# Performance work log

Measured on AMD Instinct MI355X. Metric: run time of the kernel, lower is better.

The kernel has to match this reference:

```python
import jax, jax.numpy as jnp
import numpy as np

N_EMBD = 1024
N_HEAD = 16
HEAD_SIZE = 64
EPS = 1e-5


def _layer_norm(x, gamma, beta, eps=EPS):
    mu = jnp.mean(x, axis=-1, keepdims=True)
    var = jnp.mean(jnp.square(x - mu), axis=-1, keepdims=True)
    return (x - mu) * jax.lax.rsqrt(var + eps) * gamma + beta


def setup_inputs() -> dict:
    key = jax.random.key(0)
    ks = jax.random.split(key, 10)
    C = N_EMBD
    s = 1.0 / np.sqrt(C)
    x = jax.random.normal(ks[0], (4, 2048, C), dtype=jnp.float32)
    Wq = jax.random.normal(ks[1], (C, C), dtype=jnp.float32) * s
    Wk = jax.random.normal(ks[2], (C, C), dtype=jnp.float32) * s
    Wv = jax.random.normal(ks[3], (C, C), dtype=jnp.float32) * s
    Wo = jax.random.normal(ks[4], (C, C), dtype=jnp.float32) * s
    W1 = jax.random.normal(ks[5], (C, 4 * C), dtype=jnp.float32) * s
    b1 = jnp.zeros((4 * C,), dtype=jnp.float32)
    W2 = jax.random.normal(ks[6], (4 * C, C), dtype=jnp.float32) * (1.0 / np.sqrt(4 * C))
    b2 = jnp.zeros((C,), dtype=jnp.float32)
    g1 = jnp.ones((C,), dtype=jnp.float32)
    be1 = jnp.zeros((C,), dtype=jnp.float32)
    g2 = jnp.ones((C,), dtype=jnp.float32)
    be2 = jnp.zeros((C,), dtype=jnp.float32)
    return {"x": x, "Wq": Wq, "Wk": Wk, "Wv": Wv, "Wo": Wo,
            "W1": W1, "b1": b1, "W2": W2, "b2": b2,
            "g1": g1, "be1": be1, "g2": g2, "be2": be2}


def _block(x, Wq, Wk, Wv, Wo, W1, b1, W2, b2, g1, be1, g2, be2):
    B, T, C = x.shape
    H, D = N_HEAD, HEAD_SIZE
    # attention sub-block
    h = _layer_norm(x, g1, be1)
    q = (h @ Wq.T).reshape(B, T, H, D).transpose(0, 2, 1, 3)  # [B,H,T,D]
    k = (h @ Wk.T).reshape(B, T, H, D).transpose(0, 2, 1, 3)
    v = (h @ Wv.T).reshape(B, T, H, D).transpose(0, 2, 1, 3)
    wei = jnp.einsum("bhqd,bhkd->bhqk", q, k) * (D ** -0.5)
    causal = jnp.tril(jnp.ones((T, T), dtype=bool))
    wei = jnp.where(causal, wei, -jnp.inf)
    wei = jax.nn.softmax(wei, axis=-1)
    out = jnp.einsum("bhqk,bhkd->bhqd", wei, v)
    out = out.transpose(0, 2, 1, 3).reshape(B, T, C)
    x = x + out @ Wo.T
    # FFN sub-block (exact erf GELU, matching torch default)
    h2 = _layer_norm(x, g2, be2)
    ff = jax.nn.gelu(h2 @ W1 + b1, approximate=False) @ W2 + b2
    return x + ff


def reference(x, Wq, Wk, Wv, Wo, W1, b1, W2, b2, g1, be1, g2, be2):
    return _block(x, Wq, Wk, Wv, Wo, W1, b1, W2, b2, g1, be1, g2, be2)
```

## Files before the change

### kernel.cpp

```cpp
#include <hip/hip_runtime.h>
#include <cmath>

typedef unsigned short u16;
typedef __attribute__((ext_vector_type(8))) short bf16x8;
typedef __attribute__((ext_vector_type(4))) float f32x4;

#define TT 2048
#define CC 1024
#define BT 8192

__device__ __forceinline__ float fexp2(float x) {
  return __builtin_amdgcn_exp2f(x);
}

__device__ __forceinline__ u16 f2bf(float f) {
  unsigned u = __builtin_bit_cast(unsigned, f);
  u += 0x7fffu + ((u >> 16) & 1u);
  return (u16)(u >> 16);
}

__device__ __forceinline__ float bf2f(u16 u) {
  return __builtin_bit_cast(float, (unsigned)u << 16);
}

__device__ __forceinline__ float gelu_tanh(float v) {
  float u2 = v * (1.595769122f + 0.071354816f * v * v);
  return v / (1.f + __expf(-u2));
}

__device__ __forceinline__ void gload_lds16(const void* g, void* l) {
  __builtin_amdgcn_global_load_lds(
      (const __attribute__((address_space(1))) void*)g,
      (__attribute__((address_space(3))) void*)l, 16, 0, 0);
}


__global__ __launch_bounds__(256) void cvt_kernel(const float* __restrict__ s,
                                                  u16* __restrict__ d) {
  int i = (blockIdx.x * 256 + threadIdx.x) * 4;
  float4 v = *(const float4*)(s + i);
  ushort4 o;
  o.x = f2bf(v.x); o.y = f2bf(v.y); o.z = f2bf(v.z); o.w = f2bf(v.w);
  *(ushort4*)(d + i) = o;
}

__global__ __launch_bounds__(256) void transpose_cvt(const float* __restrict__ src,
                                                     u16* __restrict__ dst,
                                                     int R, int C) {
  __shared__ float tile[32][33];
  int c0 = blockIdx.x * 32, r0 = blockIdx.y * 32;
  int tx = threadIdx.x, ty = threadIdx.y;
#pragma unroll
  for (int j = 0; j < 4; ++j)
    tile[ty + j * 8][tx] = src[(size_t)(r0 + ty + j * 8) * C + c0 + tx];
  __syncthreads();
#pragma unroll
  for (int j = 0; j < 4; ++j)
    dst[(size_t)(c0 + ty + j * 8) * R + r0 + tx] = f2bf(tile[tx][ty + j * 8]);
}


__global__ __launch_bounds__(256) void ln_kernel(const float* __restrict__ x,
                                                 const float* __restrict__ gw,
                                                 const float* __restrict__ bw,
                                                 u16* __restrict__ out) {
  int row = blockIdx.x;
  int tid = threadIdx.x;
  const size_t base = (size_t)row * CC;
  float4 v = *(const float4*)(x + base + tid * 4);
  float s = v.x + v.y + v.z + v.w;
  float q = v.x * v.x + v.y * v.y + v.z * v.z + v.w * v.w;
#pragma unroll
  for (int o = 32; o > 0; o >>= 1) {
    s += __shfl_down(s, o, 64);
    q += __shfl_down(q, o, 64);
  }
  __shared__ float red[8];
  __shared__ float stat[2];
  int lane = tid & 63, wid = tid >> 6;
  if (!lane) { red[wid] = s; red[4 + wid] = q; }
  __syncthreads();
  if (!tid) {
    float S = red[0] + red[1] + red[2] + red[3];
    float Q = red[4] + red[5] + red[6] + red[7];
    float mu = S * (1.0f / CC);
    float var = Q * (1.0f / CC) - mu * mu;
    stat[0] = mu;
    stat[1] = rsqrtf(var + 1e-5f);
  }
  __syncthreads();
  float mu = stat[0], rs = stat[1];
  int c = tid * 4;
  float4 gv = *(const float4*)(gw + c);
  float4 bv = *(const float4*)(bw + c);
  ushort4 o;
  o.x = f2bf((v.x - mu) * rs * gv.x + bv.x);
  o.y = f2bf((v.y - mu) * rs * gv.y + bv.y);
  o.z = f2bf((v.z - mu) * rs * gv.z + bv.z);
  o.w = f2bf((v.w - mu) * rs * gv.w + bv.w);
  *(ushort4*)(out + base + c) = o;
}


__global__ __launch_bounds__(256) void rf2_kernel(const u16* __restrict__ p0,
                                                  const u16* __restrict__ p1,
                                                  const float* __restrict__ b2,
                                                  const float* __restrict__ resid,
                                                  float* __restrict__ out) {
  int c = threadIdx.x * 4;
  size_t i = (size_t)blockIdx.x * CC + c;
  ushort4 a = *(const ushort4*)(p0 + i);
  ushort4 b = *(const ushort4*)(p1 + i);
  float4 r = *(const float4*)(resid + i);
  float4 bb = *(const float4*)(b2 + c);
  float4 o;
  o.x = bf2f(a.x) + bf2f(b.x) + r.x + bb.x;
  o.y = bf2f(a.y) + bf2f(b.y) + r.y + bb.y;
  o.z = bf2f(a.z) + bf2f(b.z) + r.z + bb.z;
  o.w = bf2f(a.w) + bf2f(b.w) + r.w + bb.w;
  *(float4*)(out + i) = o;
}


template <int EPI>
__global__ __launch_bounds__(512) void gemm256(const u16* __restrict__ A,
                                               const u16* __restrict__ B,
                                               void* __restrict__ Cv,
                                               const float* __restrict__ bias,
                                               const float* __restrict__ resid,
                                               u16* __restrict__ vt,
                                               int N, int K, int Kst,
                                               int gn, int kdiv) {
  __shared__ u16 lds[8][8192];
  const int tid = threadIdx.x, lane = tid & 63, wid = tid >> 6;
  const int nwg = gridDim.x;
  const int bid = blockIdx.x;
  const int sb = (nwg & 7) ? bid : ((bid & 7) * (nwg >> 3) + (bid >> 3));
  const int kslice = sb / kdiv, rem = sb % kdiv;
  const int tM = (rem / gn) * 256, tN = (rem % gn) * 256;
  const int wm = wid >> 2, wn = wid & 3;
  const int fr = lane & 15, g4 = lane >> 4;
  const int gsw = (g4 ^ ((fr >> 3) << 1)) * 8;
  const int srow0 = wid * 16 + (lane >> 2);
  const int scol = ((lane & 3) ^ ((lane >> 5) << 1)) * 8;
  const u16* pA = A + (size_t)kslice * K + (size_t)tM * Kst + (size_t)srow0 * Kst + scol;
  const u16* pB = B + (size_t)kslice * K + (size_t)tN * Kst + (size_t)srow0 * Kst + scol;
  const int NKT = K >> 6;
  f32x4 acc[8][4] = {};

  auto stage = [&](int idx) {
    int kof = (idx >> 1) << 5;
    const u16* G = (idx & 1) ? pB : pA;
    u16* dst = &lds[idx & 7][wid * 512];
    gload_lds16(G + kof, dst);
    gload_lds16(G + (size_t)128 * Kst + kof, dst + 4096);
  };

#pragma unroll
  for (int j = 0; j < 4; ++j) stage(j);
  asm volatile("s_waitcnt vmcnt(4)" ::: "memory");
#pragma unroll
  for (int j = 4; j < 7; ++j) stage(j);
  asm volatile("s_waitcnt vmcnt(6)" ::: "memory");
  __builtin_amdgcn_s_barrier();

  for (int t2 = 0; t2 < NKT; t2 += 2) {
#pragma unroll
    for (int tt = 0; tt < 2; ++tt) {
      const int t = t2 + tt;
      const int bo = tt << 2;
#pragma unroll
      for (int ks = 0; ks < 2; ++ks) {
        const u16* Ah = lds[bo | (ks << 1)];
        const u16* Bh = lds[bo | (ks << 1) | 1];
        bf16x8 bfr[4];
#pragma unroll
        for (int ni = 0; ni < 4; ++ni)
          bfr[ni] = *(const bf16x8*)&Bh[(wn * 64 + ni * 16 + fr) * 32 + gsw];
#pragma unroll
        for (int mh = 0; mh < 2; ++mh) {
          bf16x8 af[4];
#pragma unroll
          for (int mi = 0; mi < 4; ++mi)
            af[mi] = *(const bf16x8*)&Ah[(wm * 128 + mh * 64 + mi * 16 + fr) * 32 + gsw];
          __builtin_amdgcn_sched_barrier(0);
          int idx = 4 * t + (ks << 1) + mh + 7;
          if (idx < 4 * NKT) stage(idx);
          __builtin_amdgcn_s_barrier();
          asm volatile("s_waitcnt lgkmcnt(0)" ::: "memory");
          __builtin_amdgcn_sched_barrier(0);
          __builtin_amdgcn_s_setprio(1);
#pragma unroll
          for (int mi = 0; mi < 4; ++mi)
#pragma unroll
            for (int ni = 0; ni < 4; ++ni)
              acc[mh * 4 + mi][ni] = __builtin_amdgcn_mfma_f32_16x16x32_bf16(
                  af[mi], bfr[ni], acc[mh * 4 + mi][ni], 0, 0, 0);
          __builtin_amdgcn_s_setprio(0);
          __builtin_amdgcn_sched_barrier(0);
          if (ks == 1 && mh == 1) {
            if (t < NKT - 2) asm volatile("s_waitcnt vmcnt(6)" ::: "memory");
            else if (t == NKT - 2) asm volatile("s_waitcnt vmcnt(0)" ::: "memory");
          }
          __builtin_amdgcn_s_barrier();
        }
      }
    }
  }

#pragma unroll
  for (int m = 0; m < 8; ++m) {
#pragma unroll
    for (int ni = 0; ni < 4; ++ni) {
      const int gR0 = tM + wm * 128 + m * 16 + g4 * 4;
      const int gC = tN + wn * 64 + ni * 16 + fr;
      if constexpr (EPI == 4) {
        if (gC < 2048) {
          float sc = (gC < 1024) ? 0.180336884f : 1.0f;
#pragma unroll
          for (int r = 0; r < 4; ++r)
            ((u16*)Cv)[(size_t)(gR0 + r) * 3072 + gC] = f2bf(acc[m][ni][r] * sc);
        } else {
          int tr = gR0 & 2047, bb = gR0 >> 11;
          int dv = gC - 2048, hh = dv >> 6, dd = dv & 63;
          int k5 = tr & 31;
          int pos = ((k5 & 15) >> 2) * 8 + ((k5 >> 4) & 1) * 4;
          ushort4 q4;
          q4.x = f2bf(acc[m][ni][0]);
          q4.y = f2bf(acc[m][ni][1]);
          q4.z = f2bf(acc[m][ni][2]);
          q4.w = f2bf(acc[m][ni][3]);
          *(ushort4*)&vt[((size_t)((bb * 16 + hh) * 64 + dd)) * 2048 + (tr & ~31) + pos] = q4;
        }
      } else if constexpr (EPI == 0) {
        u16* dst = kslice ? vt : (u16*)Cv;
#pragma unroll
        for (int r = 0; r < 4; ++r)
          dst[(size_t)(gR0 + r) * N + gC] = f2bf(acc[m][ni][r]);
      } else if constexpr (EPI == 2) {
#pragma unroll
        for (int r = 0; r < 4; ++r) {
          float v = gelu_tanh(acc[m][ni][r] + bias[gC]);
          ((u16*)Cv)[(size_t)(gR0 + r) * N + gC] = f2bf(v);
        }
      } else {
#pragma unroll
        for (int r = 0; r < 4; ++r) {
          size_t idx = (size_t)(gR0 + r) * N + gC;
          float v = acc[m][ni][r] + resid[idx];
          if constexpr (EPI == 3) v += bias[gC];
          ((float*)Cv)[idx] = v;
        }
      }
    }
  }
}


__global__ __launch_bounds__(256) void attn_kernel(const u16* __restrict__ qkv,
                                                   const u16* __restrict__ vt,
                                                   u16* __restrict__ out) {
  const int bid = blockIdx.x;
  const int sb = (bid & 7) * 128 + (bid >> 3);
  const int pair = sb & 15;
  const int bh = sb >> 4;
  const int b = bh >> 4, h = bh & 15;
  const int tid = threadIdx.x, lane = tid & 63, wid = tid >> 6;
  const int ql = lane & 15, g = lane >> 4;
  const int sw = ql & 7;
  __shared__ u16 Ks[2][4096];
  __shared__ u16 Vs[2][4096];
  const size_t rowQbase = (size_t)b * TT;
  const u16* kpart = qkv + rowQbase * 3072 + 1024 + h * 64;
  const u16* vpart = vt + ((size_t)(b * 16 + h) * 64) * 2048;
  const int srow = lane >> 3;
  const int sc16 = lane & 7;

  for (int pass = 0; pass < 2; ++pass) {
    const int qt = pass ? (31 - pair) : pair;
    const int qrow0 = qt * 64 + wid * 16;
    const int q_glb = qrow0 + ql;
    const u16* qp = qkv + (rowQbase + q_glb) * 3072 + h * 64 + g * 8;
    bf16x8 qf0 = *(const bf16x8*)qp;
    bf16x8 qf1 = *(const bf16x8*)(qp + 32);
    f32x4 o[4] = {};
    float m_run = -1e30f, l_run = 0.f;
    const int nt = qt + 1;

    auto stage = [&](int bufi, int t) {
      int kv0 = t * 64;
#pragma unroll
      for (int i = 0; i < 2; ++i) {
        int seg = wid * 2 + i;
        int rloc = seg * 8 + srow;
        int cs = (sc16 ^ (rloc & 7)) * 8;
        gload_lds16(kpart + (size_t)(kv0 + rloc) * 3072 + cs, &Ks[bufi][seg * 512]);
        gload_lds16(vpart + (size_t)rloc * 2048 + kv0 + cs, &Vs[bufi][seg * 512]);
      }
    };

    stage(0, 0);
    __syncthreads();
    int buf = 0;
    for (int t = 0; t < nt; ++t) {
      if (t + 1 < nt) stage(buf ^ 1, t + 1);
      const u16* Kb = Ks[buf];
      const u16* Vb = Vs[buf];
      const int kv0 = t * 64;
      float p[16];
      __builtin_amdgcn_s_setprio(1);
#pragma unroll
      for (int kt = 0; kt < 4; ++kt) {
        int row = kt * 16 + ql;
        bf16x8 k0 = *(const bf16x8*)&Kb[row * 64 + ((g ^ sw) * 8)];
        bf16x8 k1 = *(const bf16x8*)&Kb[row * 64 + (((4 + g) ^ sw) * 8)];
        f32x4 s = {0.f, 0.f, 0.f, 0.f};
        s = __builtin_amdgcn_mfma_f32_16x16x32_bf16(k0, qf0, s, 0, 0, 0);
        s = __builtin_amdgcn_mfma_f32_16x16x32_bf16(k1, qf1, s, 0, 0, 0);
        if (t == qt) {
#pragma unroll
          for (int r = 0; r < 4; ++r) {
            int k_glb = kv0 + kt * 16 + 4 * g + r;
            p[kt * 4 + r] = (k_glb <= q_glb) ? s[r] : -1e30f;
          }
        } else {
#pragma unroll
          for (int r = 0; r < 4; ++r) p[kt * 4 + r] = s[r];
        }
      }
      __builtin_amdgcn_s_setprio(0);
      float t8[8];
#pragma unroll
      for (int i = 0; i < 8; ++i) t8[i] = fmaxf(p[i], p[i + 8]);
#pragma unroll
      for (int i = 0; i < 4; ++i) t8[i] = fmaxf(t8[i], t8[i + 4]);
      float mloc = fmaxf(fmaxf(t8[0], t8[1]), fmaxf(t8[2], t8[3]));
      mloc = fmaxf(mloc, __shfl_xor(mloc, 16));
      mloc = fmaxf(mloc, __shfl_xor(mloc, 32));
      if (!__all(mloc <= m_run + 8.f)) {
        float mnew = fmaxf(m_run, mloc);
        float alpha = fexp2(m_run - mnew);
        m_run = mnew;
        l_run *= alpha;
        float aO[4];
#pragma unroll
        for (int r = 0; r < 4; ++r) aO[r] = __shfl(alpha, 4 * g + r);
#pragma unroll
        for (int d0 = 0; d0 < 4; ++d0)
#pragma unroll
          for (int r = 0; r < 4; ++r) o[d0][r] *= aO[r];
      }
      float e[16];
#pragma unroll
      for (int i = 0; i < 16; ++i) e[i] = fexp2(p[i] - m_run);
      float s8[8];
#pragma unroll
      for (int i = 0; i < 8; ++i) s8[i] = e[i] + e[i + 8];
#pragma unroll
      for (int i = 0; i < 4; ++i) s8[i] += s8[i + 4];
      float lloc = (s8[0] + s8[1]) + (s8[2] + s8[3]);
      lloc += __shfl_xor(lloc, 16);
      lloc += __shfl_xor(lloc, 32);
      l_run += lloc;
      int4 w0, w1;
      asm("v_cvt_pk_bf16_f32 %0, %1, %2" : "=v"(w0.x) : "v"(e[0]), "v"(e[1]));
      asm("v_cvt_pk_bf16_f32 %0, %1, %2" : "=v"(w0.y) : "v"(e[2]), "v"(e[3]));
      asm("v_cvt_pk_bf16_f32 %0, %1, %2" : "=v"(w0.z) : "v"(e[4]), "v"(e[5]));
      asm("v_cvt_pk_bf16_f32 %0, %1, %2" : "=v"(w0.w) : "v"(e[6]), "v"(e[7]));
      asm("v_cvt_pk_bf16_f32 %0, %1, %2" : "=v"(w1.x) : "v"(e[8]), "v"(e[9]));
      asm("v_cvt_pk_bf16_f32 %0, %1, %2" : "=v"(w1.y) : "v"(e[10]), "v"(e[11]));
      asm("v_cvt_pk_bf16_f32 %0, %1, %2" : "=v"(w1.z) : "v"(e[12]), "v"(e[13]));
      asm("v_cvt_pk_bf16_f32 %0, %1, %2" : "=v"(w1.w) : "v"(e[14]), "v"(e[15]));
      bf16x8 pa0 = __builtin_bit_cast(bf16x8, w0);
      bf16x8 pa1 = __builtin_bit_cast(bf16x8, w1);
      __builtin_amdgcn_s_setprio(1);
#pragma unroll
      for (int d0 = 0; d0 < 4; ++d0) {
        int row = d0 * 16 + ql;
        bf16x8 v0 = *(const bf16x8*)&Vb[row * 64 + ((g ^ sw) * 8)];
        bf16x8 v1 = *(const bf16x8*)&Vb[row * 64 + (((4 + g) ^ sw) * 8)];
        o[d0] = __builtin_amdgcn_mfma_f32_16x16x32_bf16(pa0, v0, o[d0], 0, 0, 0);
        o[d0] = __builtin_amdgcn_mfma_f32_16x16x32_bf16(pa1, v1, o[d0], 0, 0, 0);
      }
      __builtin_amdgcn_s_setprio(0);
      __syncthreads();
      buf ^= 1;
    }
    float linv = 1.0f / l_run;
    float lO[4];
#pragma unroll
    for (int r = 0; r < 4; ++r) lO[r] = __shfl(linv, 4 * g + r);
#pragma unroll
    for (int d0 = 0; d0 < 4; ++d0) {
#pragma unroll
      for (int r = 0; r < 4; ++r) {
        size_t idx = (rowQbase + qrow0 + 4 * g + r) * CC + h * 64 + d0 * 16 + ql;
        out[idx] = f2bf(o[d0][r] * lO[r]);
      }
    }
  }
}


extern "C" void kernel_launch(void* const* d_in, const int* in_sizes, int n_in,
                              void* d_out, int out_size, void* d_ws, size_t ws_size,
                              hipStream_t stream) {
  const float* x   = (const float*)d_in[0];
  const float* Wq  = (const float*)d_in[1];
  const float* Wk  = (const float*)d_in[2];
  const float* Wv  = (const float*)d_in[3];
  const float* Wo  = (const float*)d_in[4];
  const float* W1  = (const float*)d_in[5];
  const float* b1  = (const float*)d_in[6];
  const float* W2  = (const float*)d_in[7];
  const float* b2  = (const float*)d_in[8];
  const float* g1  = (const float*)d_in[9];
  const float* be1 = (const float*)d_in[10];
  const float* g2  = (const float*)d_in[11];
  const float* be2 = (const float*)d_in[12];

  char* ws = (char*)d_ws;
  size_t off = 0;
  u16* Wqkv = (u16*)(ws + off); off += (size_t)3072 * 1024 * 2;
  u16* Wob  = (u16*)(ws + off); off += (size_t)1024 * 1024 * 2;
  u16* W1T  = (u16*)(ws + off); off += (size_t)4096 * 1024 * 2;
  u16* W2T  = (u16*)(ws + off); off += (size_t)1024 * 4096 * 2;
  u16* Hb   = (u16*)(ws + off); off += (size_t)BT * 1024 * 2;
  u16* QKV  = (u16*)(ws + off); off += (size_t)BT * 3072 * 2;
  u16* AttO = (u16*)(ws + off); off += (size_t)BT * 1024 * 2;
  float* X2 = (float*)(ws + off); off += (size_t)BT * 1024 * 4;
  u16* FF1 = QKV;
  u16* VT  = (u16*)X2;
  if (ws_size < off) return;
  const int KBIG = 1 << 20;

  cvt_kernel<<<1024, 256, 0, stream>>>(Wq, Wqkv);
  cvt_kernel<<<1024, 256, 0, stream>>>(Wk, Wqkv + 1024 * 1024);
  cvt_kernel<<<1024, 256, 0, stream>>>(Wv, Wqkv + 2 * 1024 * 1024);
  cvt_kernel<<<1024, 256, 0, stream>>>(Wo, Wob);
  transpose_cvt<<<dim3(128, 32), dim3(32, 8), 0, stream>>>(W1, W1T, 1024, 4096);
  transpose_cvt<<<dim3(32, 128), dim3(32, 8), 0, stream>>>(W2, W2T, 4096, 1024);

  ln_kernel<<<BT, 256, 0, stream>>>(x, g1, be1, Hb);
  gemm256<4><<<32 * 12, 512, 0, stream>>>(Hb, Wqkv, QKV, nullptr, nullptr, VT,
                                          3072, 1024, 1024, 12, KBIG);
  attn_kernel<<<1024, 256, 0, stream>>>(QKV, VT, AttO);
  gemm256<1><<<32 * 4, 512, 0, stream>>>(AttO, Wob, X2, nullptr, x, nullptr,
                                         1024, 1024, 1024, 4, KBIG);
  ln_kernel<<<BT, 256, 0, stream>>>(X2, g2, be2, Hb);
  gemm256<2><<<32 * 16, 512, 0, stream>>>(Hb, W1T, FF1, b1, nullptr, nullptr,
                                          4096, 1024, 1024, 16, KBIG);
  gemm256<0><<<32 * 8, 512, 0, stream>>>(FF1, W2T, Hb, nullptr, nullptr, AttO,
                                         1024, 2048, 4096, 4, 128);
  rf2_kernel<<<BT, 256, 0, stream>>>(Hb, AttO, b2, X2, (float*)d_out);
}
```

Measured before the change: 389.8 us.

## Pair two N-tiles per workgroup in FFN1 GEMM to fill one wave of CUs

Adds a PAIR mode to the 256x256 GEMM in which each workgroup computes two adjacent 256-column output tiles in sequence. The K pipeline runs continuously across both tiles, with a mid-loop epilogue and accumulator reset when the first tile finishes. The FFN1 GEMM launch drops from 512 to 256 workgroups, matching the CU count, to avoid a partial second wave and keep the load pipeline warm between tiles. The cost is a longer per-workgroup critical path, and the extra epilogue code may raise register pressure.

Result: no change. 391.5 us (+0.4%).

```diff
diff --git a/kernel.cpp b/kernel.cpp
--- a/kernel.cpp
+++ b/kernel.cpp
@@ -122,7 +122,7 @@
 }
 
 
-template <int EPI>
+template <int EPI, bool PAIR>
 __global__ __launch_bounds__(512) void gemm256(const u16* __restrict__ A,
                                                const u16* __restrict__ B,
                                                void* __restrict__ Cv,
@@ -136,8 +136,17 @@
   const int nwg = gridDim.x;
   const int bid = blockIdx.x;
   const int sb = (nwg & 7) ? bid : ((bid & 7) * (nwg >> 3) + (bid >> 3));
-  const int kslice = sb / kdiv, rem = sb % kdiv;
-  const int tM = (rem / gn) * 256, tN = (rem % gn) * 256;
+  int tM, tN, kslice;
+  if constexpr (PAIR) {
+    kslice = 0;
+    tM = (sb >> 3) * 256;
+    tN = (sb & 7) * 512;
+  } else {
+    kslice = sb / kdiv;
+    const int rem = sb % kdiv;
+    tM = (rem / gn) * 256;
+    tN = (rem % gn) * 256;
+  }
   const int wm = wid >> 2, wn = wid & 3;
   const int fr = lane & 15, g4 = lane >> 4;
   const int gsw = (g4 ^ ((fr >> 3) << 1)) * 8;
@@ -145,17 +154,69 @@
   const int scol = ((lane & 3) ^ ((lane >> 5) << 1)) * 8;
   const u16* pA = A + (size_t)kslice * K + (size_t)tM * Kst + (size_t)srow0 * Kst + scol;
   const u16* pB = B + (size_t)kslice * K + (size_t)tN * Kst + (size_t)srow0 * Kst + scol;
+  const u16* pB1 = PAIR ? (pB + (size_t)256 * Kst) : pB;
   const int NKT = K >> 6;
+  const int TNKT = PAIR ? 2 * NKT : NKT;
   f32x4 acc[8][4] = {};
 
   auto stage = [&](int idx) {
-    int kof = (idx >> 1) << 5;
-    const u16* G = (idx & 1) ? pB : pA;
+    int li = PAIR ? (idx & 63) : idx;
+    int kof = (li >> 1) << 5;
+    const u16* G = (idx & 1) ? ((PAIR && idx >= 64) ? pB1 : pB) : pA;
     u16* dst = &lds[idx & 7][wid * 512];
     gload_lds16(G + kof, dst);
     gload_lds16(G + (size_t)128 * Kst + kof, dst + 4096);
   };
 
+  auto epi = [&](int tNx) {
+#pragma unroll
+    for (int m = 0; m < 8; ++m) {
+#pragma unroll
+      for (int ni = 0; ni < 4; ++ni) {
+        const int gR0 = tM + wm * 128 + m * 16 + g4 * 4;
+        const int gC = tNx + wn * 64 + ni * 16 + fr;
+        if constexpr (EPI == 4) {
+          if (gC < 2048) {
+            float sc = (gC < 1024) ? 0.180336884f : 1.0f;
+#pragma unroll
+            for (int r = 0; r < 4; ++r)
+              ((u16*)Cv)[(size_t)(gR0 + r) * 3072 + gC] = f2bf(acc[m][ni][r] * sc);
+          } else {
+            int tr = gR0 & 2047, bb = gR0 >> 11;
+            int dv = gC - 2048, hh = dv >> 6, dd = dv & 63;
+            int k5 = tr & 31;
+            int pos = ((k5 & 15) >> 2) * 8 + ((k5 >> 4) & 1) * 4;
+            ushort4 q4;
+            q4.x = f2bf(acc[m][ni][0]);
+            q4.y = f2bf(acc[m][ni][1]);
+            q4.z = f2bf(acc[m][ni][2]);
+            q4.w = f2bf(acc[m][ni][3]);
+            *(ushort4*)&vt[((size_t)((bb * 16 + hh) * 64 + dd)) * 2048 + (tr & ~31) + pos] = q4;
+          }
+        } else if constexpr (EPI == 0) {
+          u16* dst = kslice ? vt : (u16*)Cv;
+#pragma unroll
+          for (int r = 0; r < 4; ++r)
+            dst[(size_t)(gR0 + r) * N + gC] = f2bf(acc[m][ni][r]);
+        } else if constexpr (EPI == 2) {
+#pragma unroll
+          for (int r = 0; r < 4; ++r) {
+            float v = gelu_tanh(acc[m][ni][r] + bias[gC]);
+            ((u16*)Cv)[(size_t)(gR0 + r) * N + gC] = f2bf(v);
+          }
+        } else {
+#pragma unroll
+          for (int r = 0; r < 4; ++r) {
+            size_t idx = (size_t)(gR0 + r) * N + gC;
+            float v = acc[m][ni][r] + resid[idx];
+            if constexpr (EPI == 3) v += bias[gC];
+            ((float*)Cv)[idx] = v;
+          }
+        }
+      }
+    }
+  };
+
 #pragma unroll
   for (int j = 0; j < 4; ++j) stage(j);
   asm volatile("s_waitcnt vmcnt(4)" ::: "memory");
@@ -164,7 +225,7 @@
   asm volatile("s_waitcnt vmcnt(6)" ::: "memory");
   __builtin_amdgcn_s_barrier();
 
-  for (int t2 = 0; t2 < NKT; t2 += 2) {
+  for (int t2 = 0; t2 < TNKT; t2 += 2) {
 #pragma unroll
     for (int tt = 0; tt < 2; ++tt) {
       const int t = t2 + tt;
@@ -185,7 +246,7 @@
             af[mi] = *(const bf16x8*)&Ah[(wm * 128 + mh * 64 + mi * 16 + fr) * 32 + gsw];
           __builtin_amdgcn_sched_barrier(0);
           int idx = 4 * t + (ks << 1) + mh + 7;
-          if (idx < 4 * NKT) stage(idx);
+          if (idx < 4 * TNKT) stage(idx);
           __builtin_amdgcn_s_barrier();
           asm volatile("s_waitcnt lgkmcnt(0)" ::: "memory");
           __builtin_amdgcn_sched_barrier(0);
@@ -199,61 +260,27 @@
           __builtin_amdgcn_s_setprio(0);
           __builtin_amdgcn_sched_barrier(0);
           if (ks == 1 && mh == 1) {
-            if (t < NKT - 2) asm volatile("s_waitcnt vmcnt(6)" ::: "memory");
-            else if (t == NKT - 2) asm volatile("s_waitcnt vmcnt(0)" ::: "memory");
+            if (t < TNKT - 2) asm volatile("s_waitcnt vmcnt(6)" ::: "memory");
+            else if (t == TNKT - 2) asm volatile("s_waitcnt vmcnt(0)" ::: "memory");
           }
           __builtin_amdgcn_s_barrier();
         }
       }
     }
-  }
-
-#pragma unroll
-  for (int m = 0; m < 8; ++m) {
-#pragma unroll
-    for (int ni = 0; ni < 4; ++ni) {
-      const int gR0 = tM + wm * 128 + m * 16 + g4 * 4;
-      const int gC = tN + wn * 64 + ni * 16 + fr;
-      if constexpr (EPI == 4) {
-        if (gC < 2048) {
-          float sc = (gC < 1024) ? 0.180336884f : 1.0f;
-#pragma unroll
-          for (int r = 0; r < 4; ++r)
-            ((u16*)Cv)[(size_t)(gR0 + r) * 3072 + gC] = f2bf(acc[m][ni][r] * sc);
-        } else {
-          int tr = gR0 & 2047, bb = gR0 >> 11;
-          int dv = gC - 2048, hh = dv >> 6, dd = dv & 63;
-          int k5 = tr & 31;
-          int pos = ((k5 & 15) >> 2) * 8 + ((k5 >> 4) & 1) * 4;
-          ushort4 q4;
-          q4.x = f2bf(acc[m][ni][0]);
-          q4.y = f2bf(acc[m][ni][1]);
-          q4.z = f2bf(acc[m][ni][2]);
-          q4.w = f2bf(acc[m][ni][3]);
-          *(ushort4*)&vt[((size_t)((bb * 16 + hh) * 64 + dd)) * 2048 + (tr & ~31) + pos] = q4;
-        }
-      } else if constexpr (EPI == 0) {
-        u16* dst = kslice ? vt : (u16*)Cv;
-#pragma unroll
-        for (int r = 0; r < 4; ++r)
-          dst[(size_t)(gR0 + r) * N + gC] = f2bf(acc[m][ni][r]);
-      } else if constexpr (EPI == 2) {
-#pragma unroll
-        for (int r = 0; r < 4; ++r) {
-          float v = gelu_tanh(acc[m][ni][r] + bias[gC]);
-          ((u16*)Cv)[(size_t)(gR0 + r) * N + gC] = f2bf(v);
-        }
-      } else {
-#pragma unroll
-        for (int r = 0; r < 4; ++r) {
-          size_t idx = (size_t)(gR0 + r) * N + gC;
-          float v = acc[m][ni][r] + resid[idx];
-          if constexpr (EPI == 3) v += bias[gC];
-          ((float*)Cv)[idx] = v;
-        }
+    if constexpr (PAIR) {
+      if (t2 + 2 == NKT) {
+        epi(tN);
+        tN += 256;
+        f32x4 z = {0.f, 0.f, 0.f, 0.f};
+#pragma unroll
+        for (int m = 0; m < 8; ++m)
+#pragma unroll
+          for (int ni = 0; ni < 4; ++ni) acc[m][ni] = z;
       }
     }
   }
+
+  epi(tN);
 }
 
 
@@ -442,15 +469,15 @@
   transpose_cvt<<<dim3(32, 128), dim3(32, 8), 0, stream>>>(W2, W2T, 4096, 1024);
 
   ln_kernel<<<BT, 256, 0, stream>>>(x, g1, be1, Hb);
-  gemm256<4><<<32 * 12, 512, 0, stream>>>(Hb, Wqkv, QKV, nullptr, nullptr, VT,
-                                          3072, 1024, 1024, 12, KBIG);
+  gemm256<4, false><<<32 * 12, 512, 0, stream>>>(Hb, Wqkv, QKV, nullptr, nullptr, VT,
+                                                 3072, 1024, 1024, 12, KBIG);
   attn_kernel<<<1024, 256, 0, stream>>>(QKV, VT, AttO);
-  gemm256<1><<<32 * 4, 512, 0, stream>>>(AttO, Wob, X2, nullptr, x, nullptr,
-                                         1024, 1024, 1024, 4, KBIG);
+  gemm256<1, false><<<32 * 4, 512, 0, stream>>>(AttO, Wob, X2, nullptr, x, nullptr,
+                                                1024, 1024, 1024, 4, KBIG);
   ln_kernel<<<BT, 256, 0, stream>>>(X2, g2, be2, Hb);
-  gemm256<2><<<32 * 16, 512, 0, stream>>>(Hb, W1T, FF1, b1, nullptr, nullptr,
-                                          4096, 1024, 1024, 16, KBIG);
-  gemm256<0><<<32 * 8, 512, 0, stream>>>(FF1, W2T, Hb, nullptr, nullptr, AttO,
-                                         1024, 2048, 4096, 4, 128);
+  gemm256<2, true><<<256, 512, 0, stream>>>(Hb, W1T, FF1, b1, nullptr, nullptr,
+                                            4096, 1024, 1024, 16, KBIG);
+  gemm256<0, false><<<32 * 8, 512, 0, stream>>>(FF1, W2T, Hb, nullptr, nullptr, AttO,
+                                                1024, 2048, 4096, 4, 128);
   rf2_kernel<<<BT, 256, 0, stream>>>(Hb, AttO, b2, X2, (float*)d_out);
 }
```

## Process paired causal query tiles together in attention and merge weight-cast launches

Applied to the files above, without the earlier changes.

The attention kernel used to handle its two query tiles (pair and 31-pair) in two passes, and each pass re-streamed K/V from tile 0. Now it keeps both query tiles' state live and makes a single pass over K/V, so each staged K/V tile is shared by both. The lower tile is processed only while it is still inside its causal range. This roughly halves K/V staging and barriers for mid-range pairs and adds independent MFMA chains, at the cost of twice the accumulator and Q registers, which may reduce occupancy. Separately, the four Wq/Wk/Wv/Wo bf16 conversion launches are merged into one kernel that writes contiguous output.

Result: slower. 410.9 us (+5.4%).

```diff
diff --git a/kernel.cpp b/kernel.cpp
--- a/kernel.cpp
+++ b/kernel.cpp
@@ -35,13 +35,19 @@
 }
 
 
-__global__ __launch_bounds__(256) void cvt_kernel(const float* __restrict__ s,
-                                                  u16* __restrict__ d) {
-  int i = (blockIdx.x * 256 + threadIdx.x) * 4;
+__global__ __launch_bounds__(256) void cvt4_kernel(const float* __restrict__ s0,
+                                                   const float* __restrict__ s1,
+                                                   const float* __restrict__ s2,
+                                                   const float* __restrict__ s3,
+                                                   u16* __restrict__ d) {
+  int blk = blockIdx.x;
+  int seg = blk >> 10;
+  const float* s = (seg == 0) ? s0 : (seg == 1) ? s1 : (seg == 2) ? s2 : s3;
+  int i = ((blk & 1023) * 256 + threadIdx.x) * 4;
   float4 v = *(const float4*)(s + i);
   ushort4 o;
   o.x = f2bf(v.x); o.y = f2bf(v.y); o.z = f2bf(v.z); o.w = f2bf(v.w);
-  *(ushort4*)(d + i) = o;
+  *(ushort4*)(d + (seg << 20) + i) = o;
 }
 
 __global__ __launch_bounds__(256) void transpose_cvt(const float* __restrict__ src,
@@ -276,116 +282,127 @@
   const int srow = lane >> 3;
   const int sc16 = lane & 7;
 
-  for (int pass = 0; pass < 2; ++pass) {
-    const int qt = pass ? (31 - pair) : pair;
-    const int qrow0 = qt * 64 + wid * 16;
-    const int q_glb = qrow0 + ql;
-    const u16* qp = qkv + (rowQbase + q_glb) * 3072 + h * 64 + g * 8;
-    bf16x8 qf0 = *(const bf16x8*)qp;
-    bf16x8 qf1 = *(const bf16x8*)(qp + 32);
-    f32x4 o[4] = {};
-    float m_run = -1e30f, l_run = 0.f;
-    const int nt = qt + 1;
-
-    auto stage = [&](int bufi, int t) {
-      int kv0 = t * 64;
-#pragma unroll
-      for (int i = 0; i < 2; ++i) {
-        int seg = wid * 2 + i;
-        int rloc = seg * 8 + srow;
-        int cs = (sc16 ^ (rloc & 7)) * 8;
-        gload_lds16(kpart + (size_t)(kv0 + rloc) * 3072 + cs, &Ks[bufi][seg * 512]);
-        gload_lds16(vpart + (size_t)rloc * 2048 + kv0 + cs, &Vs[bufi][seg * 512]);
+  const int qa = pair, qb = 31 - pair;
+  const int qrow0a = qa * 64 + wid * 16;
+  const int qrow0b = qb * 64 + wid * 16;
+  const u16* qpa = qkv + (rowQbase + qrow0a + ql) * 3072 + h * 64 + g * 8;
+  const u16* qpb = qkv + (rowQbase + qrow0b + ql) * 3072 + h * 64 + g * 8;
+  bf16x8 qf0a = *(const bf16x8*)qpa;
+  bf16x8 qf1a = *(const bf16x8*)(qpa + 32);
+  bf16x8 qf0b = *(const bf16x8*)qpb;
+  bf16x8 qf1b = *(const bf16x8*)(qpb + 32);
+  f32x4 oa[4] = {}, ob[4] = {};
+  float ma = -1e30f, la = 0.f, mb = -1e30f, lb = 0.f;
+  const int nt = qb + 1;
+
+  auto stage = [&](int bufi, int t) {
+    int kv0 = t * 64;
+#pragma unroll
+    for (int i = 0; i < 2; ++i) {
+      int seg = wid * 2 + i;
+      int rloc = seg * 8 + srow;
+      int cs = (sc16 ^ (rloc & 7)) * 8;
+      gload_lds16(kpart + (size_t)(kv0 + rloc) * 3072 + cs, &Ks[bufi][seg * 512]);
+      gload_lds16(vpart + (size_t)rloc * 2048 + kv0 + cs, &Vs[bufi][seg * 512]);
+    }
+  };
+
+  auto process = [&](const u16* Kb, const u16* Vb, int t, int qt, int q_glb,
+                     bf16x8 qf0, bf16x8 qf1, f32x4 (&o)[4],
+                     float& m_run, float& l_run) {
+    const int kv0 = t * 64;
+    float p[16];
+    __builtin_amdgcn_s_setprio(1);
+#pragma unroll
+    for (int kt = 0; kt < 4; ++kt) {
+      int row = kt * 16 + ql;
+      bf16x8 k0 = *(const bf16x8*)&Kb[row * 64 + ((g ^ sw) * 8)];
+      bf16x8 k1 = *(const bf16x8*)&Kb[row * 64 + (((4 + g) ^ sw) * 8)];
+      f32x4 s = {0.f, 0.f, 0.f, 0.f};
+      s = __builtin_amdgcn_mfma_f32_16x16x32_bf16(k0, qf0, s, 0, 0, 0);
+      s = __builtin_amdgcn_mfma_f32_16x16x32_bf16(k1, qf1, s, 0, 0, 0);
+      if (t == qt) {
+#pragma unroll
+        for (int r = 0; r < 4; ++r) {
+          int k_glb = kv0 + kt * 16 + 4 * g + r;
+          p[kt * 4 + r] = (k_glb <= q_glb) ? s[r] : -1e30f;
+        }
+      } else {
+#pragma unroll
+        for (int r = 0; r < 4; ++r) p[kt * 4 + r] = s[r];
       }
-    };
-
-    stage(0, 0);
+    }
+    __builtin_amdgcn_s_setprio(0);
+    float t8[8];
+#pragma unroll
+    for (int i = 0; i < 8; ++i) t8[i] = fmaxf(p[i], p[i + 8]);
+#pragma unroll
+    for (int i = 0; i < 4; ++i) t8[i] = fmaxf(t8[i], t8[i + 4]);
+    float mloc = fmaxf(fmaxf(t8[0], t8[1]), fmaxf(t8[2], t8[3]));
+    mloc = fmaxf(mloc, __shfl_xor(mloc, 16));
+    mloc = fmaxf(mloc, __shfl_xor(mloc, 32));
+    if (!__all(mloc <= m_run + 8.f)) {
+      float mnew = fmaxf(m_run, mloc);
+      float alpha = fexp2(m_run - mnew);
+      m_run = mnew;
+      l_run *= alpha;
+      float aO[4];
+#pragma unroll
+      for (int r = 0; r < 4; ++r) aO[r] = __shfl(alpha, 4 * g + r);
+#pragma unroll
+      for (int d0 = 0; d0 < 4; ++d0)
+#pragma unroll
+        for (int r = 0; r < 4; ++r) o[d0][r] *= aO[r];
+    }
+    float e[16];
+#pragma unroll
+    for (int i = 0; i < 16; ++i) e[i] = fexp2(p[i] - m_run);
+    float s8[8];
+#pragma unroll
+    for (int i = 0; i < 8; ++i) s8[i] = e[i] + e[i + 8];
+#pragma unroll
+    for (int i = 0; i < 4; ++i) s8[i] += s8[i + 4];
+    float lloc = (s8[0] + s8[1]) + (s8[2] + s8[3]);
+    lloc += __shfl_xor(lloc, 16);
+    lloc += __shfl_xor(lloc, 32);
+    l_run += lloc;
+    int4 w0, w1;
+    asm("v_cvt_pk_bf16_f32 %0, %1, %2" : "=v"(w0.x) : "v"(e[0]), "v"(e[1]));
+    asm("v_cvt_pk_bf16_f32 %0, %1, %2" : "=v"(w0.y) : "v"(e[2]), "v"(e[3]));
+    asm("v_cvt_pk_bf16_f32 %0, %1, %2" : "=v"(w0.z) : "v"(e[4]), "v"(e[5]));
+    asm("v_cvt_pk_bf16_f32 %0, %1, %2" : "=v"(w0.w) : "v"(e[6]), "v"(e[7]));
+    asm("v_cvt_pk_bf16_f32 %0, %1, %2" : "=v"(w1.x) : "v"(e[8]), "v"(e[9]));
+    asm("v_cvt_pk_bf16_f32 %0, %1, %2" : "=v"(w1.y) : "v"(e[10]), "v"(e[11]));
+    asm("v_cvt_pk_bf16_f32 %0, %1, %2" : "=v"(w1.z) : "v"(e[12]), "v"(e[13]));
+    asm("v_cvt_pk_bf16_f32 %0, %1, %2" : "=v"(w1.w) : "v"(e[14]), "v"(e[15]));
+    bf16x8 pa0 = __builtin_bit_cast(bf16x8, w0);
+    bf16x8 pa1 = __builtin_bit_cast(bf16x8, w1);
+    __builtin_amdgcn_s_setprio(1);
+#pragma unroll
+    for (int d0 = 0; d0 < 4; ++d0) {
+      int row = d0 * 16 + ql;
+      bf16x8 v0 = *(const bf16x8*)&Vb[row * 64 + ((g ^ sw) * 8)];
+      bf16x8 v1 = *(const bf16x8*)&Vb[row * 64 + (((4 + g) ^ sw) * 8)];
+      o[d0] = __builtin_amdgcn_mfma_f32_16x16x32_bf16(pa0, v0, o[d0], 0, 0, 0);
+      o[d0] = __builtin_amdgcn_mfma_f32_16x16x32_bf16(pa1, v1, o[d0], 0, 0, 0);
+    }
+    __builtin_amdgcn_s_setprio(0);
+  };
+
+  stage(0, 0);
+  __syncthreads();
+  int buf = 0;
+  for (int t = 0; t < nt; ++t) {
+    if (t + 1 < nt) stage(buf ^ 1, t + 1);
+    const u16* Kb = Ks[buf];
+    const u16* Vb = Vs[buf];
+    if (t <= qa) process(Kb, Vb, t, qa, qrow0a + ql, qf0a, qf1a, oa, ma, la);
+    process(Kb, Vb, t, qb, qrow0b + ql, qf0b, qf1b, ob, mb, lb);
     __syncthreads();
-    int buf = 0;
-    for (int t = 0; t < nt; ++t) {
-      if (t + 1 < nt) stage(buf ^ 1, t + 1);
-      const u16* Kb = Ks[buf];
-      const u16* Vb = Vs[buf];
-      const int kv0 = t * 64;
-      float p[16];
-      __builtin_amdgcn_s_setprio(1);
-#pragma unroll
-      for (int kt = 0; kt < 4; ++kt) {
-        int row = kt * 16 + ql;
-        bf16x8 k0 = *(const bf16x8*)&Kb[row * 64 + ((g ^ sw) * 8)];
-        bf16x8 k1 = *(const bf16x8*)&Kb[row * 64 + (((4 + g) ^ sw) * 8)];
-        f32x4 s = {0.f, 0.f, 0.f, 0.f};
-        s = __builtin_amdgcn_mfma_f32_16x16x32_bf16(k0, qf0, s, 0, 0, 0);
-        s = __builtin_amdgcn_mfma_f32_16x16x32_bf16(k1, qf1, s, 0, 0, 0);
-        if (t == qt) {
-#pragma unroll
-          for (int r = 0; r < 4; ++r) {
-            int k_glb = kv0 + kt * 16 + 4 * g + r;
-            p[kt * 4 + r] = (k_glb <= q_glb) ? s[r] : -1e30f;
-          }
-        } else {
-#pragma unroll
-          for (int r = 0; r < 4; ++r) p[kt * 4 + r] = s[r];
-        }
-      }
-      __builtin_amdgcn_s_setprio(0);
-      float t8[8];
-#pragma unroll
-      for (int i = 0; i < 8; ++i) t8[i] = fmaxf(p[i], p[i + 8]);
-#pragma unroll
-      for (int i = 0; i < 4; ++i) t8[i] = fmaxf(t8[i], t8[i + 4]);
-      float mloc = fmaxf(fmaxf(t8[0], t8[1]), fmaxf(t8[2], t8[3]));
-      mloc = fmaxf(mloc, __shfl_xor(mloc, 16));
-      mloc = fmaxf(mloc, __shfl_xor(mloc, 32));
-      if (!__all(mloc <= m_run + 8.f)) {
-        float mnew = fmaxf(m_run, mloc);
-        float alpha = fexp2(m_run - mnew);
-        m_run = mnew;
-        l_run *= alpha;
-        float aO[4];
-#pragma unroll
-        for (int r = 0; r < 4; ++r) aO[r] = __shfl(alpha, 4 * g + r);
-#pragma unroll
-        for (int d0 = 0; d0 < 4; ++d0)
-#pragma unroll
-          for (int r = 0; r < 4; ++r) o[d0][r] *= aO[r];
-      }
-      float e[16];
-#pragma unroll
-      for (int i = 0; i < 16; ++i) e[i] = fexp2(p[i] - m_run);
-      float s8[8];
-#pragma unroll
-      for (int i = 0; i < 8; ++i) s8[i] = e[i] + e[i + 8];
-#pragma unroll
-      for (int i = 0; i < 4; ++i) s8[i] += s8[i + 4];
-      float lloc = (s8[0] + s8[1]) + (s8[2] + s8[3]);
-      lloc += __shfl_xor(lloc, 16);
-      lloc += __shfl_xor(lloc, 32);
-      l_run += lloc;
-      int4 w0, w1;
-      asm("v_cvt_pk_bf16_f32 %0, %1, %2" : "=v"(w0.x) : "v"(e[0]), "v"(e[1]));
-      asm("v_cvt_pk_bf16_f32 %0, %1, %2" : "=v"(w0.y) : "v"(e[2]), "v"(e[3]));
-      asm("v_cvt_pk_bf16_f32 %0, %1, %2" : "=v"(w0.z) : "v"(e[4]), "v"(e[5]));
-      asm("v_cvt_pk_bf16_f32 %0, %1, %2" : "=v"(w0.w) : "v"(e[6]), "v"(e[7]));
-      asm("v_cvt_pk_bf16_f32 %0, %1, %2" : "=v"(w1.x) : "v"(e[8]), "v"(e[9]));
-      asm("v_cvt_pk_bf16_f32 %0, %1, %2" : "=v"(w1.y) : "v"(e[10]), "v"(e[11]));
-      asm("v_cvt_pk_bf16_f32 %0, %1, %2" : "=v"(w1.z) : "v"(e[12]), "v"(e[13]));
-      asm("v_cvt_pk_bf16_f32 %0, %1, %2" : "=v"(w1.w) : "v"(e[14]), "v"(e[15]));
-      bf16x8 pa0 = __builtin_bit_cast(bf16x8, w0);
-      bf16x8 pa1 = __builtin_bit_cast(bf16x8, w1);
-      __builtin_amdgcn_s_setprio(1);
-#pragma unroll
-      for (int d0 = 0; d0 < 4; ++d0) {
-        int row = d0 * 16 + ql;
-        bf16x8 v0 = *(const bf16x8*)&Vb[row * 64 + ((g ^ sw) * 8)];
-        bf16x8 v1 = *(const bf16x8*)&Vb[row * 64 + (((4 + g) ^ sw) * 8)];
-        o[d0] = __builtin_amdgcn_mfma_f32_16x16x32_bf16(pa0, v0, o[d0], 0, 0, 0);
-        o[d0] = __builtin_amdgcn_mfma_f32_16x16x32_bf16(pa1, v1, o[d0], 0, 0, 0);
-      }
-      __builtin_amdgcn_s_setprio(0);
-      __syncthreads();
-      buf ^= 1;
-    }
+    buf ^= 1;
+  }
+
+  auto writeout = [&](f32x4 (&o)[4], float l_run, int qrow0) {
     float linv = 1.0f / l_run;
     float lO[4];
 #pragma unroll
@@ -398,7 +415,9 @@
         out[idx] = f2bf(o[d0][r] * lO[r]);
       }
     }
-  }
+  };
+  writeout(oa, la, qrow0a);
+  writeout(ob, lb, qrow0b);
 }
 
 
@@ -434,10 +453,7 @@
   if (ws_size < off) return;
   const int KBIG = 1 << 20;
 
-  cvt_kernel<<<1024, 256, 0, stream>>>(Wq, Wqkv);
-  cvt_kernel<<<1024, 256, 0, stream>>>(Wk, Wqkv + 1024 * 1024);
-  cvt_kernel<<<1024, 256, 0, stream>>>(Wv, Wqkv + 2 * 1024 * 1024);
-  cvt_kernel<<<1024, 256, 0, stream>>>(Wo, Wob);
+  cvt4_kernel<<<4096, 256, 0, stream>>>(Wq, Wk, Wv, Wo, Wqkv);
   transpose_cvt<<<dim3(128, 32), dim3(32, 8), 0, stream>>>(W1, W1T, 1024, 4096);
   transpose_cvt<<<dim3(32, 128), dim3(32, 8), 0, stream>>>(W2, W2T, 4096, 1024);
 
```
